# Optimization experiments

Measured on AMD Instinct MI355X. Metric: run time of the kernel, lower is better.

Reference implementation:

```python
import jax, jax.numpy as jnp
import numpy as np

EPS = 1e-5
HEADS = 4


def _ln(x, s, b):
    m = jnp.mean(x, axis=-1, keepdims=True)
    v = jnp.mean(jnp.square(x - m), axis=-1, keepdims=True)
    return (x - m) * jax.lax.rsqrt(v + EPS) * s + b


def _gru(x, Wg, bg, Wcx, bcx, Wch, bch):
    # In this GRUCell the gates depend only on the inputs, so the gate and
    # candidate_x matmuls are precomputed over all timesteps; only the
    # (reset*h) @ Wch matmul is sequential.
    gx = jax.nn.sigmoid(x @ Wg + bg)   # [B,S,2H]
    cx = x @ Wcx + bcx                 # [B,S,H]
    H = Wch.shape[0]

    def step(h, gc):
        g, c = gc
        r, u = jnp.split(g, 2, axis=-1)
        cand = jnp.tanh(c + (r * h) @ Wch + bch)
        h_new = u * h + (1.0 - u) * cand
        return h_new, h_new

    h0 = jnp.zeros((x.shape[0], H), x.dtype)
    _, ys = jax.lax.scan(step, h0, (gx.transpose(1, 0, 2), cx.transpose(1, 0, 2)))
    return ys.transpose(1, 0, 2)


def _attn(x, s, b, Wq, bq, Wk, bk, Wv, bv, Wo, bo):
    skip = x
    xn = _ln(x, s, b)
    B, S, _ = xn.shape
    QKV = Wq.shape[1]
    hd = QKV // HEADS
    q = (xn @ Wq + bq).reshape(B, S, HEADS, hd)
    k = (xn @ Wk + bk).reshape(B, S, HEADS, hd)
    v = (xn @ Wv + bv).reshape(B, S, HEADS, hd)
    scores = jnp.einsum('bqhd,bkhd->bhqk', q, k) / jnp.sqrt(jnp.asarray(hd, x.dtype))
    probs = jax.nn.softmax(scores, axis=-1)
    o = jnp.einsum('bhqk,bkhd->bqhd', probs, v).reshape(B, S, QKV)
    return o @ Wo + bo + skip


def _forward(x_cgm, x_other, W_in, b_in, ln0_s, ln0_b,
             g0_Wg, g0_bg, g0_Wcx, g0_bcx, g0_Wch, g0_bch, ln1_s, ln1_b,
             g1_Wg, g1_bg, g1_Wcx, g1_bcx, g1_Wch, g1_bch, ln2_s, ln2_b,
             aln_s, aln_b, Wq, bq, Wk, bk, Wv, bv, Wo, bo,
             Wd1, bd1, lnd1_s, lnd1_b, Wd2, bd2, lnd2_s, lnd2_b, Wout, bout):
    # input projection + LN
    x = _ln(x_cgm @ W_in + b_in, ln0_s, ln0_b)
    # GRU block 0 (residual: dims match, 256==256)
    y = _gru(x, g0_Wg, g0_bg, g0_Wcx, g0_bcx, g0_Wch, g0_bch)
    x = _ln(y, ln1_s, ln1_b) + x
    # GRU block 1
    y = _gru(x, g1_Wg, g1_bg, g1_Wcx, g1_bcx, g1_Wch, g1_bch)
    x = _ln(y, ln2_s, ln2_b) + x
    # attention block after every 2nd GRU block
    x = _attn(x, aln_s, aln_b, Wq, bq, Wk, bk, Wv, bv, Wo, bo)
    # pool over time, concat static features, dense head (no residuals: dims differ)
    pooled = jnp.mean(x, axis=1)
    c = jnp.concatenate([pooled, x_other], axis=-1)
    c = _ln(jax.nn.relu(c @ Wd1 + bd1), lnd1_s, lnd1_b)
    c = _ln(jax.nn.relu(c @ Wd2 + bd2), lnd2_s, lnd2_b)
    return (c @ Wout + bout).squeeze(-1)


def setup_inputs() -> dict:
    key = jax.random.key(0)
    ks = iter(jax.random.split(key, 64))

    def nrm(shape, scale=1.0):
        return jax.random.normal(next(ks), shape, jnp.float32) * scale

    B, S, Fc, Fo, D, QKV = 64, 288, 16, 32, 256, 64
    inp = {
        'x_cgm': nrm((B, S, Fc)),
        'x_other': nrm((B, Fo)),
        'W_in': nrm((Fc, D), Fc ** -0.5), 'b_in': jnp.zeros((D,), jnp.float32),
        'ln0_s': jnp.ones((D,), jnp.float32), 'ln0_b': jnp.zeros((D,), jnp.float32),
    }
    for p in ('g0', 'g1'):
        inp[p + '_Wg'] = nrm((D, 2 * D), D ** -0.5)
        inp[p + '_bg'] = jnp.zeros((2 * D,), jnp.float32)
        inp[p + '_Wcx'] = nrm((D, D), D ** -0.5)
        inp[p + '_bcx'] = jnp.zeros((D,), jnp.float32)
        inp[p + '_Wch'] = nrm((D, D), D ** -0.5)
        inp[p + '_bch'] = jnp.zeros((D,), jnp.float32)
    for n in ('ln1', 'ln2', 'aln'):
        inp[n + '_s'] = jnp.ones((D,), jnp.float32)
        inp[n + '_b'] = jnp.zeros((D,), jnp.float32)
    for n in ('Wq', 'Wk', 'Wv'):
        inp[n] = nrm((D, QKV), D ** -0.5)
    for n in ('bq', 'bk', 'bv'):
        inp[n] = jnp.zeros((QKV,), jnp.float32)
    inp['Wo'] = nrm((QKV, D), QKV ** -0.5)
    inp['bo'] = jnp.zeros((D,), jnp.float32)
    inp['Wd1'] = nrm((D + Fo, 128), (D + Fo) ** -0.5)
    inp['bd1'] = jnp.zeros((128,), jnp.float32)
    inp['lnd1_s'] = jnp.ones((128,), jnp.float32)
    inp['lnd1_b'] = jnp.zeros((128,), jnp.float32)
    inp['Wd2'] = nrm((128, 64), 128 ** -0.5)
    inp['bd2'] = jnp.zeros((64,), jnp.float32)
    inp['lnd2_s'] = jnp.ones((64,), jnp.float32)
    inp['lnd2_b'] = jnp.zeros((64,), jnp.float32)
    inp['Wout'] = nrm((64, 1), 64 ** -0.5)
    inp['bout'] = jnp.zeros((1,), jnp.float32)
    return inp


def reference(x_cgm, x_other, W_in, b_in, ln0_s, ln0_b,
              g0_Wg, g0_bg, g0_Wcx, g0_bcx, g0_Wch, g0_bch, ln1_s, ln1_b,
              g1_Wg, g1_bg, g1_Wcx, g1_bcx, g1_Wch, g1_bch, ln2_s, ln2_b,
              aln_s, aln_b, Wq, bq, Wk, bk, Wv, bv, Wo, bo,
              Wd1, bd1, lnd1_s, lnd1_b, Wd2, bd2, lnd2_s, lnd2_b, Wout, bout):
    return _forward(x_cgm, x_other, W_in, b_in, ln0_s, ln0_b,
                    g0_Wg, g0_bg, g0_Wcx, g0_bcx, g0_Wch, g0_bch, ln1_s, ln1_b,
                    g1_Wg, g1_bg, g1_Wcx, g1_bcx, g1_Wch, g1_bch, ln2_s, ln2_b,
                    aln_s, aln_b, Wq, bq, Wk, bk, Wv, bv, Wo, bo,
                    Wd1, bd1, lnd1_s, lnd1_b, Wd2, bd2, lnd2_s, lnd2_b, Wout, bout)
```

## Files before the change

### kernel.cpp

```cpp
#include <hip/hip_runtime.h>
#include <hip/hip_bf16.h>
#include <math.h>


#define EPS 1e-5f
constexpr int B_ = 64, S_ = 288, FC = 16, FO = 32, D_ = 256, QKVN = 64, HD = 16;
constexpr int TOK = B_ * S_;
constexpr int NX = TOK * D_;
constexpr int NG = TOK * 512;

typedef short bf16x8 __attribute__((ext_vector_type(8)));
typedef float f32x4 __attribute__((ext_vector_type(4)));

__device__ __forceinline__ short f2bf(float f) {
  __hip_bfloat16 h = __float2bfloat16(f);
  return __builtin_bit_cast(short, h);
}

__device__ __forceinline__ float blk_sum(float v, float* sc) {
  #pragma unroll
  for (int o = 32; o > 0; o >>= 1) v += __shfl_down(v, o, 64);
  int tid = threadIdx.x;
  int wid = tid >> 6, nw = blockDim.x >> 6;
  __syncthreads();
  if ((tid & 63) == 0) sc[wid] = v;
  __syncthreads();
  float s = 0.f;
  for (int w = 0; w < nw; ++w) s += sc[w];
  return s;
}

__global__ __launch_bounds__(256) void inproj_ln(
    const float* __restrict__ xc, const float* __restrict__ Wi,
    const float* __restrict__ bi, const float* __restrict__ sc_,
    const float* __restrict__ bb, float* __restrict__ X) {
  __shared__ float sc[8];
  int tok = blockIdx.x, j = threadIdx.x;
  const float* xr = xc + tok * FC;
  float acc = bi[j];
  #pragma unroll
  for (int i = 0; i < FC; ++i) acc += xr[i] * Wi[i * D_ + j];
  float m = blk_sum(acc, sc) * (1.f / D_);
  float d = acc - m;
  float var = blk_sum(d * d, sc) * (1.f / D_);
  X[tok * D_ + j] = d * rsqrtf(var + EPS) * sc_[j] + bb[j];
}

template <int RES>
__global__ __launch_bounds__(256) void ln_token(
    const float* __restrict__ in, const float* __restrict__ sc_,
    const float* __restrict__ bb, const float* __restrict__ resid,
    float* __restrict__ out) {
  __shared__ float sc[8];
  int tok = blockIdx.x, j = threadIdx.x;
  float v = in[tok * D_ + j];
  float m = blk_sum(v, sc) * (1.f / D_);
  float d = v - m;
  float var = blk_sum(d * d, sc) * (1.f / D_);
  float r = d * rsqrtf(var + EPS) * sc_[j] + bb[j];
  if (RES) r += resid[tok * D_ + j];
  out[tok * D_ + j] = r;
}

template <int BN, int ACT, int RES>
__global__ __launch_bounds__(256) void gemm_mfma(
    const float* __restrict__ A, const float* __restrict__ W,
    const float* __restrict__ bias, const float* __restrict__ resid,
    float* __restrict__ OUT, int K, int N) {
  constexpr int BM = 128, BK = 32;
  constexpr int NT16 = BN / 16;
  constexpr int BTASK = BN * 4 / 256;
  __shared__ short As[BM * 40];
  __shared__ short Bs[BN * 40];
  int tid = threadIdx.x;
  int wave = tid >> 6, lane = tid & 63;
  int quad = lane >> 4, m16 = lane & 15;
  int row0 = blockIdx.x * BM;
  int bn0 = blockIdx.y * BN;

  f32x4 acc[2][NT16];
  #pragma unroll
  for (int mt = 0; mt < 2; ++mt)
    #pragma unroll
    for (int nt = 0; nt < NT16; ++nt) acc[mt][nt] = (f32x4){0.f, 0.f, 0.f, 0.f};

  const float* Ag = A + (size_t)row0 * K;

  for (int kk = 0; kk < K; kk += BK) {
    __syncthreads();
    #pragma unroll
    for (int i = 0; i < 4; ++i) {
      int t = tid + i * 256;
      int r = t >> 3, kq = t & 7;
      float4 a4 = *(const float4*)(Ag + (size_t)r * K + kk + kq * 4);
      short4 s4 = make_short4(f2bf(a4.x), f2bf(a4.y), f2bf(a4.z), f2bf(a4.w));
      *(short4*)&As[r * 40 + kq * 4] = s4;
    }
    #pragma unroll
    for (int i = 0; i < BTASK; ++i) {
      int t = tid + i * 256;
      int n = t % BN, oct = t / BN;
      const float* bp = W + (size_t)(kk + oct * 8) * N + bn0 + n;
      bf16x8 bv;
      #pragma unroll
      for (int j = 0; j < 8; ++j) bv[j] = f2bf(bp[(size_t)j * N]);
      *(bf16x8*)&Bs[n * 40 + oct * 8] = bv;
    }
    __syncthreads();
    bf16x8 af0 = *(const bf16x8*)&As[(wave * 32 + m16) * 40 + quad * 8];
    bf16x8 af1 = *(const bf16x8*)&As[(wave * 32 + 16 + m16) * 40 + quad * 8];
    #pragma unroll
    for (int nt = 0; nt < NT16; ++nt) {
      bf16x8 bfr = *(const bf16x8*)&Bs[(nt * 16 + m16) * 40 + quad * 8];
      acc[0][nt] = __builtin_amdgcn_mfma_f32_16x16x32_bf16(af0, bfr, acc[0][nt], 0, 0, 0);
      acc[1][nt] = __builtin_amdgcn_mfma_f32_16x16x32_bf16(af1, bfr, acc[1][nt], 0, 0, 0);
    }
  }
  #pragma unroll
  for (int mt = 0; mt < 2; ++mt) {
    #pragma unroll
    for (int nt = 0; nt < NT16; ++nt) {
      int col = bn0 + nt * 16 + m16;
      float bv = bias[col];
      #pragma unroll
      for (int r = 0; r < 4; ++r) {
        int row = row0 + wave * 32 + mt * 16 + quad * 4 + r;
        float v = acc[mt][nt][r] + bv;
        if (ACT == 1) v = 1.f / (1.f + __expf(-v));
        if (RES) v += resid[(size_t)row * N + col];
        OUT[(size_t)row * N + col] = v;
      }
    }
  }
}

__global__ __launch_bounds__(512, 2) void gru_scan(
    const float* __restrict__ G, const float* __restrict__ C,
    const float* __restrict__ Wch, const float* __restrict__ bch,
    float* __restrict__ Y) {
  __shared__ short vstage[256];
  int tid = threadIdx.x;
  int b = blockIdx.x;
  int wave = tid >> 6, lane = tid & 63;
  int quad = lane >> 4, m16 = lane & 15;
  int col0 = 32 * wave + m16;
  int col1 = col0 + 16;

  bf16x8 wfrag[2][8];
  #pragma unroll
  for (int tt = 0; tt < 2; ++tt) {
    int n = (tt == 0) ? col0 : col1;
    #pragma unroll
    for (int c = 0; c < 8; ++c) {
      const float* wp = Wch + (size_t)(32 * c + quad * 8) * D_ + n;
      bf16x8 w;
      #pragma unroll
      for (int j = 0; j < 8; ++j) w[j] = f2bf(wp[(size_t)j * D_]);
      wfrag[tt][c] = w;
    }
  }

  const float* Gp = G + (size_t)b * S_ * 512;
  const float* Cp = C + (size_t)b * S_ * 256;
  float* Yp = Y + (size_t)b * S_ * 256;

  float bch0 = bch[col0], bch1 = bch[col1];
  float h0 = 0.f, h1 = 0.f;
  float u0 = Gp[256 + col0], u1 = Gp[256 + col1];
  float c0 = Cp[col0], c1 = Cp[col1];
  float r0n = Gp[512 + col0], r1n = Gp[512 + col1];

  if (tid < 256) vstage[tid] = 0;
  __syncthreads();

  for (int t = 0; t < S_; ++t) {
    f32x4 acc0 = {0.f, 0.f, 0.f, 0.f}, acc1 = {0.f, 0.f, 0.f, 0.f};
    #pragma unroll
    for (int c = 0; c < 8; ++c) {
      bf16x8 af = *(const bf16x8*)&vstage[(c * 4 + quad) * 8];
      acc0 = __builtin_amdgcn_mfma_f32_16x16x32_bf16(af, wfrag[0][c], acc0, 0, 0, 0);
      acc1 = __builtin_amdgcn_mfma_f32_16x16x32_bf16(af, wfrag[1][c], acc1, 0, 0, 0);
    }
    float u0n = 0.f, u1n = 0.f, c0n = 0.f, c1n = 0.f, r0nn = 0.f, r1nn = 0.f;
    if (t + 1 < S_) {
      size_t bn = (size_t)(t + 1);
      u0n = Gp[bn * 512 + 256 + col0]; u1n = Gp[bn * 512 + 256 + col1];
      c0n = Cp[bn * 256 + col0];       c1n = Cp[bn * 256 + col1];
    }
    if (t + 2 < S_) {
      size_t b2 = (size_t)(t + 2);
      r0nn = Gp[b2 * 512 + col0];      r1nn = Gp[b2 * 512 + col1];
    }
    float s0 = c0 + bch0 + acc0[0];
    float s1 = c1 + bch1 + acc1[0];
    float e0 = __expf(2.f * s0), e1 = __expf(2.f * s1);
    float cand0 = 1.f - 2.f / (e0 + 1.f);
    float cand1 = 1.f - 2.f / (e1 + 1.f);
    h0 = u0 * h0 + (1.f - u0) * cand0;
    h1 = u1 * h1 + (1.f - u1) * cand1;
    short v0 = f2bf(r0n * h0), v1 = f2bf(r1n * h1);
    __syncthreads();
    if (quad == 0) {
      Yp[(size_t)t * 256 + col0] = h0;
      Yp[(size_t)t * 256 + col1] = h1;
      vstage[col0] = v0;
      vstage[col1] = v1;
    }
    u0 = u0n; u1 = u1n; c0 = c0n; c1 = c1n; r0n = r0nn; r1n = r1nn;
    __syncthreads();
  }
}

__global__ __launch_bounds__(320) void attn(
    const float* __restrict__ Q, const float* __restrict__ Kv,
    const float* __restrict__ V, float* __restrict__ AO) {
  __shared__ float Kl[S_ * HD];
  __shared__ float Vl[S_ * HD];
  int b = blockIdx.x, hh = blockIdx.y;
  int tid = threadIdx.x;
  int hoff = hh * HD;
  for (int idx = tid; idx < S_ * HD; idx += 320) {
    int row = idx >> 4, d = idx & 15;
    Kl[idx] = Kv[((size_t)(b * S_ + row)) * QKVN + hoff + d];
    Vl[idx] = V[((size_t)(b * S_ + row)) * QKVN + hoff + d];
  }
  __syncthreads();
  if (tid >= S_) return;
  const float* qp = Q + ((size_t)(b * S_ + tid)) * QKVN + hoff;
  float4 q0 = *(const float4*)(qp + 0);
  float4 q1 = *(const float4*)(qp + 4);
  float4 q2 = *(const float4*)(qp + 8);
  float4 q3 = *(const float4*)(qp + 12);
  float m = -1e30f, l = 0.f;
  float4 o0 = {0, 0, 0, 0}, o1 = {0, 0, 0, 0}, o2 = {0, 0, 0, 0},
         o3 = {0, 0, 0, 0};
  for (int k = 0; k < S_; ++k) {
    const float4* kp = (const float4*)&Kl[k * HD];
    float4 k0 = kp[0], k1 = kp[1], k2 = kp[2], k3 = kp[3];
    float s = q0.x * k0.x + q0.y * k0.y + q0.z * k0.z + q0.w * k0.w +
              q1.x * k1.x + q1.y * k1.y + q1.z * k1.z + q1.w * k1.w +
              q2.x * k2.x + q2.y * k2.y + q2.z * k2.z + q2.w * k2.w +
              q3.x * k3.x + q3.y * k3.y + q3.z * k3.z + q3.w * k3.w;
    s *= 0.25f;
    float mn = fmaxf(m, s);
    float corr = __expf(m - mn);
    float p = __expf(s - mn);
    l = l * corr + p;
    const float4* vp = (const float4*)&Vl[k * HD];
    float4 v0 = vp[0], v1 = vp[1], v2 = vp[2], v3 = vp[3];
    o0.x = o0.x * corr + p * v0.x; o0.y = o0.y * corr + p * v0.y;
    o0.z = o0.z * corr + p * v0.z; o0.w = o0.w * corr + p * v0.w;
    o1.x = o1.x * corr + p * v1.x; o1.y = o1.y * corr + p * v1.y;
    o1.z = o1.z * corr + p * v1.z; o1.w = o1.w * corr + p * v1.w;
    o2.x = o2.x * corr + p * v2.x; o2.y = o2.y * corr + p * v2.y;
    o2.z = o2.z * corr + p * v2.z; o2.w = o2.w * corr + p * v2.w;
    o3.x = o3.x * corr + p * v3.x; o3.y = o3.y * corr + p * v3.y;
    o3.z = o3.z * corr + p * v3.z; o3.w = o3.w * corr + p * v3.w;
    m = mn;
  }
  float inv = 1.f / l;
  float* op = AO + ((size_t)(b * S_ + tid)) * QKVN + hoff;
  float4 r0 = {o0.x * inv, o0.y * inv, o0.z * inv, o0.w * inv};
  float4 r1 = {o1.x * inv, o1.y * inv, o1.z * inv, o1.w * inv};
  float4 r2 = {o2.x * inv, o2.y * inv, o2.z * inv, o2.w * inv};
  float4 r3 = {o3.x * inv, o3.y * inv, o3.z * inv, o3.w * inv};
  ((float4*)op)[0] = r0; ((float4*)op)[1] = r1;
  ((float4*)op)[2] = r2; ((float4*)op)[3] = r3;
}

__global__ __launch_bounds__(128) void head(
    const float* __restrict__ X, const float* __restrict__ xo,
    const float* __restrict__ Wd1, const float* __restrict__ bd1,
    const float* __restrict__ s1, const float* __restrict__ b1,
    const float* __restrict__ Wd2, const float* __restrict__ bd2,
    const float* __restrict__ s2, const float* __restrict__ b2,
    const float* __restrict__ Wout, const float* __restrict__ bout,
    float* __restrict__ out) {
  __shared__ float c[D_ + FO];
  __shared__ float h1[128];
  __shared__ float sc[8];
  int b = blockIdx.x, tid = threadIdx.x;
  for (int cc = tid; cc < D_; cc += 128) {
    float acc = 0.f;
    for (int t = 0; t < S_; ++t) acc += X[((size_t)(b * S_ + t)) * D_ + cc];
    c[cc] = acc * (1.f / S_);
  }
  if (tid < FO) c[D_ + tid] = xo[b * FO + tid];
  __syncthreads();
  float v = bd1[tid];
  for (int k = 0; k < D_ + FO; ++k) v += c[k] * Wd1[k * 128 + tid];
  v = fmaxf(v, 0.f);
  float m = blk_sum(v, sc) * (1.f / 128.f);
  float d = v - m;
  float var = blk_sum(d * d, sc) * (1.f / 128.f);
  h1[tid] = d * rsqrtf(var + EPS) * s1[tid] + b1[tid];
  __syncthreads();
  float v2 = 0.f;
  if (tid < 64) {
    v2 = bd2[tid];
    for (int k = 0; k < 128; ++k) v2 += h1[k] * Wd2[k * 64 + tid];
    v2 = fmaxf(v2, 0.f);
  }
  float m2 = blk_sum(tid < 64 ? v2 : 0.f, sc) * (1.f / 64.f);
  float d2v = v2 - m2;
  float var2 = blk_sum(tid < 64 ? d2v * d2v : 0.f, sc) * (1.f / 64.f);
  float hv = (tid < 64) ? (d2v * rsqrtf(var2 + EPS) * s2[tid] + b2[tid]) : 0.f;
  float p = (tid < 64) ? hv * Wout[tid] : 0.f;
  float tot = blk_sum(p, sc);
  if (tid == 0) out[b] = tot + bout[0];
}

extern "C" void kernel_launch(void* const* d_in, const int* in_sizes, int n_in,
                              void* d_out, int out_size, void* d_ws,
                              size_t ws_size, hipStream_t stream) {
  const float* x_cgm = (const float*)d_in[0];
  const float* x_other = (const float*)d_in[1];
  const float* W_in = (const float*)d_in[2];
  const float* b_in = (const float*)d_in[3];
  const float* ln0_s = (const float*)d_in[4];
  const float* ln0_b = (const float*)d_in[5];
  const float* g0_Wg = (const float*)d_in[6];
  const float* g0_bg = (const float*)d_in[7];
  const float* g0_Wcx = (const float*)d_in[8];
  const float* g0_bcx = (const float*)d_in[9];
  const float* g0_Wch = (const float*)d_in[10];
  const float* g0_bch = (const float*)d_in[11];
  const float* g1_Wg = (const float*)d_in[12];
  const float* g1_bg = (const float*)d_in[13];
  const float* g1_Wcx = (const float*)d_in[14];
  const float* g1_bcx = (const float*)d_in[15];
  const float* g1_Wch = (const float*)d_in[16];
  const float* g1_bch = (const float*)d_in[17];
  const float* ln1_s = (const float*)d_in[18];
  const float* ln1_b = (const float*)d_in[19];
  const float* ln2_s = (const float*)d_in[20];
  const float* ln2_b = (const float*)d_in[21];
  const float* aln_s = (const float*)d_in[22];
  const float* aln_b = (const float*)d_in[23];
  const float* Wq = (const float*)d_in[24];
  const float* Wk = (const float*)d_in[25];
  const float* Wv = (const float*)d_in[26];
  const float* bq = (const float*)d_in[27];
  const float* bk = (const float*)d_in[28];
  const float* bv = (const float*)d_in[29];
  const float* Wo = (const float*)d_in[30];
  const float* bo = (const float*)d_in[31];
  const float* Wd1 = (const float*)d_in[32];
  const float* bd1 = (const float*)d_in[33];
  const float* lnd1_s = (const float*)d_in[34];
  const float* lnd1_b = (const float*)d_in[35];
  const float* Wd2 = (const float*)d_in[36];
  const float* bd2 = (const float*)d_in[37];
  const float* lnd2_s = (const float*)d_in[38];
  const float* lnd2_b = (const float*)d_in[39];
  const float* Wout = (const float*)d_in[40];
  const float* bout = (const float*)d_in[41];
  (void)in_sizes; (void)n_in; (void)out_size; (void)ws_size;

  float* ws = (float*)d_ws;
  float* X = ws;
  float* Yb = ws + NX;
  float* Gb = ws + 2 * NX;
  float* Cb = Gb + NG;
  float* Qb = Gb;
  float* Kb = Gb + TOK * QKVN;
  float* Vb = Gb + 2 * TOK * QKVN;
  float* AO = Cb;

  const int MB = TOK / 128;

  inproj_ln<<<TOK, 256, 0, stream>>>(x_cgm, W_in, b_in, ln0_s, ln0_b, X);

  gemm_mfma<128, 1, 0><<<dim3(MB, 4), 256, 0, stream>>>(X, g0_Wg, g0_bg, nullptr, Gb, 256, 512);
  gemm_mfma<128, 0, 0><<<dim3(MB, 2), 256, 0, stream>>>(X, g0_Wcx, g0_bcx, nullptr, Cb, 256, 256);
  gru_scan<<<B_, 512, 0, stream>>>(Gb, Cb, g0_Wch, g0_bch, Yb);
  ln_token<1><<<TOK, 256, 0, stream>>>(Yb, ln1_s, ln1_b, X, X);

  gemm_mfma<128, 1, 0><<<dim3(MB, 4), 256, 0, stream>>>(X, g1_Wg, g1_bg, nullptr, Gb, 256, 512);
  gemm_mfma<128, 0, 0><<<dim3(MB, 2), 256, 0, stream>>>(X, g1_Wcx, g1_bcx, nullptr, Cb, 256, 256);
  gru_scan<<<B_, 512, 0, stream>>>(Gb, Cb, g1_Wch, g1_bch, Yb);
  ln_token<1><<<TOK, 256, 0, stream>>>(Yb, ln2_s, ln2_b, X, X);

  ln_token<0><<<TOK, 256, 0, stream>>>(X, aln_s, aln_b, nullptr, Yb);
  gemm_mfma<64, 0, 0><<<dim3(MB, 1), 256, 0, stream>>>(Yb, Wq, bq, nullptr, Qb, 256, 64);
  gemm_mfma<64, 0, 0><<<dim3(MB, 1), 256, 0, stream>>>(Yb, Wk, bk, nullptr, Kb, 256, 64);
  gemm_mfma<64, 0, 0><<<dim3(MB, 1), 256, 0, stream>>>(Yb, Wv, bv, nullptr, Vb, 256, 64);
  attn<<<dim3(B_, 4), 320, 0, stream>>>(Qb, Kb, Vb, AO);
  gemm_mfma<128, 0, 1><<<dim3(MB, 2), 256, 0, stream>>>(AO, Wo, bo, X, X, 64, 256);

  head<<<B_, 128, 0, stream>>>(X, x_other, Wd1, bd1, lnd1_s, lnd1_b,
                               Wd2, bd2, lnd2_s, lnd2_b, Wout, bout,
                               (float*)d_out);
}
```

Before: 739.4 us.

## Double-buffer GRU state in LDS, deepen gate prefetch, split MFMA accumulator chains

The GRU scan kernel now double-buffers the shared h-vector staging, which removes one of the two block barriers per timestep. Gate and candidate loads are prefetched three steps ahead through a register ring instead of one to two. The MFMA reduction over K is split into two independent accumulator chains to shorten the dependent latency. This costs extra registers and LDS, and clamps out-of-range prefetches to the last timestep.

```diff
diff --git a/kernel.cpp b/kernel.cpp
--- a/kernel.cpp
+++ b/kernel.cpp
@@ -138,7 +138,7 @@
     const float* __restrict__ G, const float* __restrict__ C,
     const float* __restrict__ Wch, const float* __restrict__ bch,
     float* __restrict__ Y) {
-  __shared__ short vstage[256];
+  __shared__ short vstage[2][256];
   int tid = threadIdx.x;
   int b = blockIdx.x;
   int wave = tid >> 6, lane = tid & 63;
@@ -166,47 +166,62 @@
 
   float bch0 = bch[col0], bch1 = bch[col1];
   float h0 = 0.f, h1 = 0.f;
-  float u0 = Gp[256 + col0], u1 = Gp[256 + col1];
-  float c0 = Cp[col0], c1 = Cp[col1];
-  float r0n = Gp[512 + col0], r1n = Gp[512 + col1];
-
-  if (tid < 256) vstage[tid] = 0;
+
+  float u0p[3], u1p[3], c0p[3], c1p[3], r0p[3], r1p[3];
+  #pragma unroll
+  for (int i = 0; i < 3; ++i) {
+    size_t ti = (size_t)i;
+    u0p[i] = Gp[ti * 512 + 256 + col0]; u1p[i] = Gp[ti * 512 + 256 + col1];
+    c0p[i] = Cp[ti * 256 + col0];       c1p[i] = Cp[ti * 256 + col1];
+    size_t tr = ti + 1;
+    r0p[i] = Gp[tr * 512 + col0];       r1p[i] = Gp[tr * 512 + col1];
+  }
+
+  if (tid < 256) vstage[0][tid] = 0;
   __syncthreads();
 
   for (int t = 0; t < S_; ++t) {
-    f32x4 acc0 = {0.f, 0.f, 0.f, 0.f}, acc1 = {0.f, 0.f, 0.f, 0.f};
-    #pragma unroll
-    for (int c = 0; c < 8; ++c) {
-      bf16x8 af = *(const bf16x8*)&vstage[(c * 4 + quad) * 8];
-      acc0 = __builtin_amdgcn_mfma_f32_16x16x32_bf16(af, wfrag[0][c], acc0, 0, 0, 0);
-      acc1 = __builtin_amdgcn_mfma_f32_16x16x32_bf16(af, wfrag[1][c], acc1, 0, 0, 0);
-    }
-    float u0n = 0.f, u1n = 0.f, c0n = 0.f, c1n = 0.f, r0nn = 0.f, r1nn = 0.f;
-    if (t + 1 < S_) {
-      size_t bn = (size_t)(t + 1);
-      u0n = Gp[bn * 512 + 256 + col0]; u1n = Gp[bn * 512 + 256 + col1];
-      c0n = Cp[bn * 256 + col0];       c1n = Cp[bn * 256 + col1];
-    }
-    if (t + 2 < S_) {
-      size_t b2 = (size_t)(t + 2);
-      r0nn = Gp[b2 * 512 + col0];      r1nn = Gp[b2 * 512 + col1];
-    }
-    float s0 = c0 + bch0 + acc0[0];
-    float s1 = c1 + bch1 + acc1[0];
+    int buf = t & 1;
+    f32x4 a0a = {0.f, 0.f, 0.f, 0.f}, a0b = {0.f, 0.f, 0.f, 0.f};
+    f32x4 a1a = {0.f, 0.f, 0.f, 0.f}, a1b = {0.f, 0.f, 0.f, 0.f};
+    #pragma unroll
+    for (int c = 0; c < 4; ++c) {
+      bf16x8 afA = *(const bf16x8*)&vstage[buf][(c * 4 + quad) * 8];
+      bf16x8 afB = *(const bf16x8*)&vstage[buf][((c + 4) * 4 + quad) * 8];
+      a0a = __builtin_amdgcn_mfma_f32_16x16x32_bf16(afA, wfrag[0][c], a0a, 0, 0, 0);
+      a1a = __builtin_amdgcn_mfma_f32_16x16x32_bf16(afA, wfrag[1][c], a1a, 0, 0, 0);
+      a0b = __builtin_amdgcn_mfma_f32_16x16x32_bf16(afB, wfrag[0][c + 4], a0b, 0, 0, 0);
+      a1b = __builtin_amdgcn_mfma_f32_16x16x32_bf16(afB, wfrag[1][c + 4], a1b, 0, 0, 0);
+    }
+    int tl = (t + 3 < S_) ? t + 3 : S_ - 1;
+    int tr = (t + 4 < S_) ? t + 4 : S_ - 1;
+    float u0n = Gp[(size_t)tl * 512 + 256 + col0];
+    float u1n = Gp[(size_t)tl * 512 + 256 + col1];
+    float c0n = Cp[(size_t)tl * 256 + col0];
+    float c1n = Cp[(size_t)tl * 256 + col1];
+    float r0n = Gp[(size_t)tr * 512 + col0];
+    float r1n = Gp[(size_t)tr * 512 + col1];
+
+    float s0 = c0p[0] + bch0 + a0a[0] + a0b[0];
+    float s1 = c1p[0] + bch1 + a1a[0] + a1b[0];
     float e0 = __expf(2.f * s0), e1 = __expf(2.f * s1);
     float cand0 = 1.f - 2.f / (e0 + 1.f);
     float cand1 = 1.f - 2.f / (e1 + 1.f);
-    h0 = u0 * h0 + (1.f - u0) * cand0;
-    h1 = u1 * h1 + (1.f - u1) * cand1;
-    short v0 = f2bf(r0n * h0), v1 = f2bf(r1n * h1);
-    __syncthreads();
+    h0 = u0p[0] * h0 + (1.f - u0p[0]) * cand0;
+    h1 = u1p[0] * h1 + (1.f - u1p[0]) * cand1;
+    short v0 = f2bf(r0p[0] * h0), v1 = f2bf(r1p[0] * h1);
     if (quad == 0) {
       Yp[(size_t)t * 256 + col0] = h0;
       Yp[(size_t)t * 256 + col1] = h1;
-      vstage[col0] = v0;
-      vstage[col1] = v1;
-    }
-    u0 = u0n; u1 = u1n; c0 = c0n; c1 = c1n; r0n = r0nn; r1n = r1nn;
+      vstage[buf ^ 1][col0] = v0;
+      vstage[buf ^ 1][col1] = v1;
+    }
+    u0p[0] = u0p[1]; u0p[1] = u0p[2]; u0p[2] = u0n;
+    u1p[0] = u1p[1]; u1p[1] = u1p[2]; u1p[2] = u1n;
+    c0p[0] = c0p[1]; c0p[1] = c0p[2]; c0p[2] = c0n;
+    c1p[0] = c1p[1]; c1p[1] = c1p[2]; c1p[2] = c1n;
+    r0p[0] = r0p[1]; r0p[1] = r0p[2]; r0p[2] = r0n;
+    r1p[0] = r1p[1]; r1p[1] = r1p[2]; r1p[2] = r1n;
     __syncthreads();
   }
 }
```

Result: slower. 782.6 us (+5.8%).
